# Performance work log

Hardware: AMD Instinct MI355X
Metric: run time of the kernel (lower is better)

The kernel has to match this reference:

```python
import jax, jax.numpy as jnp
import numpy as np
import math

B, S, D, H, R = 4, 2048, 2048, 16, 16
HD = D // H

def setup_inputs() -> dict:
    key = jax.random.key(0)
    ks = jax.random.split(key, 16)
    x = jax.random.normal(ks[0], (B, S, D), dtype=jnp.float32)
    # causal mask: 1 where attendable, 0 where masked (mask==0 -> -1e9)
    mask = jnp.tril(jnp.ones((S, S), dtype=jnp.int32))[None, None, :, :]
    def lin(k):
        return jax.random.normal(k, (D, D), dtype=jnp.float32) / math.sqrt(D)
    def lora(ka, kb):
        A = jax.random.normal(ka, (R, D), dtype=jnp.float32) / math.sqrt(D)
        Bm = jnp.zeros((D, R), dtype=jnp.float32)  # standard LoRA init: B = 0
        return A, Bm
    Aq, Bq = lora(ks[1], ks[2]); Ak, Bk = lora(ks[3], ks[4])
    Av, Bv = lora(ks[5], ks[6]); Ao, Bo = lora(ks[7], ks[8])
    return {"x": x, "mask": mask,
            "Wq": lin(ks[9]), "Aq": Aq, "Bq": Bq,
            "Wk": lin(ks[10]), "Ak": Ak, "Bk": Bk,
            "Wv": lin(ks[11]), "Av": Av, "Bv": Bv,
            "Wo": lin(ks[12]), "Ao": Ao, "Bo": Bo}

def _lora_linear(x, W, A, Bm):
    # y = x @ W^T + (x @ A^T) @ B^T   (LoRA-augmented linear, no bias)
    return x @ W.T + (x @ A.T) @ Bm.T

def reference(x, mask, Wq, Aq, Bq, Wk, Ak, Bk, Wv, Av, Bv, Wo, Ao, Bo):
    b, s, d = x.shape
    def heads(t):
        return t.reshape(b, s, H, HD).transpose(0, 2, 1, 3)  # [B,H,S,HD]
    Q = heads(_lora_linear(x, Wq, Aq, Bq))
    K = heads(_lora_linear(x, Wk, Ak, Bk))
    V = heads(_lora_linear(x, Wv, Av, Bv))
    attn = jnp.einsum('bhqd,bhkd->bhqk', Q, K) / math.sqrt(HD)
    attn = jnp.where(mask == 0, jnp.float32(-1e9), attn)
    attn = jax.nn.softmax(attn, axis=-1)
    out = jnp.einsum('bhqk,bhkd->bhqd', attn, V)  # [B,H,S,HD]
    out = out.transpose(0, 2, 1, 3).reshape(b, s, d)
    return _lora_linear(out, Wo, Ao, Bo)
```

## Files before the change

### kernel.cpp

```cpp
#include <hip/hip_runtime.h>
#include <hip/hip_bf16.h>
#include <stdint.h>


#define L2E 1.4426950408889634f
#define SMSCALE 0.08838834764831845f
#define NEGBIG -3.0e38f

typedef __attribute__((ext_vector_type(4))) float f32x4;
typedef __attribute__((ext_vector_type(16))) float f32x16;
typedef __attribute__((ext_vector_type(8))) __bf16 bfrag;

#if __has_builtin(__builtin_amdgcn_exp2f)
#define EXP2 __builtin_amdgcn_exp2f
#else
#define EXP2 exp2f
#endif

#define DRAIN_VM                                      \
  do {                                                \
    asm volatile("s_waitcnt vmcnt(0)" ::: "memory");  \
    __builtin_amdgcn_sched_barrier(0);                \
  } while (0)

static __device__ __forceinline__ unsigned short f2bf(float f) {
  union { float f; unsigned u; } v; v.f = f;
  unsigned r = v.u + 0x7FFFu + ((v.u >> 16) & 1u);
  return (unsigned short)(r >> 16);
}

static __device__ __forceinline__ void gload16(const void* g, void* l) {
  __builtin_amdgcn_global_load_lds(
      (const __attribute__((address_space(1))) void*)g,
      (__attribute__((address_space(3))) void*)l, 16, 0, 0);
}

struct F4 {
  const float* W[4];
  const float* A[4];
  const float* Bm[4];
};

__global__ __launch_bounds__(256) void k_fold4(F4 f, unsigned short* __restrict__ out) {
  const int y = blockIdx.y;
  const int n = blockIdx.x;
  const int k0 = threadIdx.x * 8;
  const float* W = f.W[y];
  const float* Aa = f.A[y];
  const float* Bm = f.Bm[y];
  const float* wr = W + (size_t)n * 2048 + k0;
  float acc[8];
#pragma unroll
  for (int j = 0; j < 8; ++j) acc[j] = wr[j];
#pragma unroll 4
  for (int r = 0; r < 16; ++r) {
    float b = Bm[n * 16 + r];
    const float* ar = Aa + (size_t)r * 2048 + k0;
#pragma unroll
    for (int j = 0; j < 8; ++j) acc[j] = fmaf(b, ar[j], acc[j]);
  }
  unsigned short o[8];
#pragma unroll
  for (int j = 0; j < 8; ++j) o[j] = f2bf(acc[j]);
  *(uint4*)(out + (((size_t)y * 2048 + n) * 2048) + k0) = *(const uint4*)o;
}

__global__ __launch_bounds__(256) void k_cvt(const float* __restrict__ in,
                                             unsigned short* __restrict__ out) {
  const size_t i = ((size_t)blockIdx.x * 256 + threadIdx.x) * 8;
  unsigned short o[8];
#pragma unroll
  for (int j = 0; j < 8; ++j) o[j] = f2bf(in[i + j]);
  *(uint4*)(out + i) = *(const uint4*)o;
}

template <int MODE>
__global__ __launch_bounds__(512, 2) void k_gemm2(const unsigned short* __restrict__ A,
                                                  const unsigned short* __restrict__ Bw,
                                                  void* __restrict__ Cout, float scale) {
  __shared__ __align__(16) unsigned char lds[131072];
  unsigned char* Al = lds;
  unsigned char* Bl = lds + 65536;
  const int tid = threadIdx.x, ln = tid & 63;
  const int w = tid >> 6, g = ln >> 4, cc = ln & 15;
  const int wm = w >> 2, wn = w & 3;
  const int bid = blockIdx.x;
  const int wg = (bid & 7) * 32 + (bid >> 3);
  const int m0 = (wg >> 3) * 256, n0 = (wg & 7) * 256;

  int soff[2], sdst[2];
#pragma unroll
  for (int i = 0; i < 2; ++i) {
    int cid = i * 512 + tid, r = cid >> 2, p = cid & 3;
    int sc = p ^ ((r >> 1) & 3);
    soff[i] = r * 2048 + sc * 8;
    sdst[i] = cid * 16;
  }
  int aro[8], bro[4];
#pragma unroll
  for (int fm = 0; fm < 8; ++fm) {
    int r = wm * 128 + fm * 16 + cc;
    aro[fm] = r * 64 + ((g ^ ((r >> 1) & 3)) << 4);
  }
#pragma unroll
  for (int fn = 0; fn < 4; ++fn) {
    int r = wn * 64 + fn * 16 + cc;
    bro[fn] = r * 64 + ((g ^ ((r >> 1) & 3)) << 4);
  }

#define STAGE_A(b, kt, h)                                                   \
  do {                                                                      \
    _Pragma("unroll")                                                       \
    for (int i = 0; i < 2; ++i)                                             \
      gload16(A + (size_t)m0 * 2048 + soff[i] + (kt) + (h) * 32,            \
              Al + (b) * 32768 + (h) * 16384 + sdst[i]);                    \
  } while (0)
#define STAGE_B(b, kt, h)                                                   \
  do {                                                                      \
    _Pragma("unroll")                                                       \
    for (int i = 0; i < 2; ++i)                                             \
      gload16(Bw + (size_t)n0 * 2048 + soff[i] + (kt) + (h) * 32,           \
              Bl + (b) * 32768 + (h) * 16384 + sdst[i]);                    \
  } while (0)

  f32x4 acc[8][4] = {};

  STAGE_A(0, 0, 0); STAGE_B(0, 0, 0);
  STAGE_A(0, 0, 1); STAGE_B(0, 0, 1);
  asm volatile("s_waitcnt vmcnt(4)" ::: "memory");
  __builtin_amdgcn_s_barrier();
  __builtin_amdgcn_sched_barrier(0);

  for (int T = 0; T < 32; ++T) {
    const int buf = T & 1;
    const unsigned char* Ab = Al + buf * 32768;
    const unsigned char* Bb = Bl + buf * 32768;
    const int ktn = (T + 1) * 64;
    const bool pf = (T + 1 < 32);
#pragma unroll
    for (int ks = 0; ks < 2; ++ks) {
      bfrag af[8], bf0[2], bf1[2];
#pragma unroll
      for (int fm = 0; fm < 8; ++fm)
        af[fm] = *(const bfrag*)(Ab + ks * 16384 + aro[fm]);
#pragma unroll
      for (int j = 0; j < 2; ++j)
        bf0[j] = *(const bfrag*)(Bb + ks * 16384 + bro[j]);
      if (pf) STAGE_A(buf ^ 1, ktn, ks);
      __builtin_amdgcn_sched_barrier(0);
      __builtin_amdgcn_s_barrier();
      asm volatile("s_waitcnt lgkmcnt(0)" ::: "memory");
      __builtin_amdgcn_sched_barrier(0);
      __builtin_amdgcn_s_setprio(1);
#pragma unroll
      for (int fm = 0; fm < 8; ++fm)
#pragma unroll
        for (int j = 0; j < 2; ++j)
          acc[fm][j] = __builtin_amdgcn_mfma_f32_16x16x32_bf16(af[fm], bf0[j],
                                                               acc[fm][j], 0, 0, 0);
      __builtin_amdgcn_s_setprio(0);
      __builtin_amdgcn_sched_barrier(0);
      __builtin_amdgcn_s_barrier();
#pragma unroll
      for (int j = 0; j < 2; ++j)
        bf1[j] = *(const bfrag*)(Bb + ks * 16384 + bro[2 + j]);
      if (pf) STAGE_B(buf ^ 1, ktn, ks);
      __builtin_amdgcn_sched_barrier(0);
      __builtin_amdgcn_s_barrier();
      asm volatile("s_waitcnt lgkmcnt(0)" ::: "memory");
      __builtin_amdgcn_sched_barrier(0);
      __builtin_amdgcn_s_setprio(1);
#pragma unroll
      for (int fm = 0; fm < 8; ++fm)
#pragma unroll
        for (int j = 0; j < 2; ++j)
          acc[fm][2 + j] = __builtin_amdgcn_mfma_f32_16x16x32_bf16(af[fm], bf1[j],
                                                                   acc[fm][2 + j], 0, 0, 0);
      __builtin_amdgcn_s_setprio(0);
      __builtin_amdgcn_sched_barrier(0);
      if (ks == 0) {
        if (T < 31) asm volatile("s_waitcnt vmcnt(4)" ::: "memory");
        else        asm volatile("s_waitcnt vmcnt(0)" ::: "memory");
      } else {
        if (T < 31) asm volatile("s_waitcnt vmcnt(4)" ::: "memory");
      }
      __builtin_amdgcn_sched_barrier(0);
      __builtin_amdgcn_s_barrier();
    }
  }
#undef STAGE_A
#undef STAGE_B

#pragma unroll
  for (int fm = 0; fm < 8; ++fm)
#pragma unroll
    for (int fn = 0; fn < 4; ++fn)
#pragma unroll
      for (int r = 0; r < 4; ++r) {
        int row = m0 + wm * 128 + fm * 16 + g * 4 + r;
        int col = n0 + wn * 64 + fn * 16 + cc;
        float v = acc[fm][fn][r];
        if (MODE == 0) {
          int b = row >> 11, s = row & 2047, h = col >> 7, hd = col & 127;
          ((unsigned short*)Cout)[(((size_t)b * 16 + h) * 2048 + s) * 128 + hd] =
              f2bf(v * scale);
        } else if (MODE == 2) {
          int b = row >> 11, s = row & 2047, h = col >> 7, hd = col & 127;
          ((unsigned short*)Cout)[(((size_t)b * 16 + h) * 128 + hd) * 2048 + s] =
              f2bf(v);
        } else {
          ((float*)Cout)[(size_t)row * 2048 + col] = v;
        }
      }
}

__global__ __launch_bounds__(512) void k_attn(const unsigned short* __restrict__ Q,
                                              const unsigned short* __restrict__ K,
                                              const unsigned short* __restrict__ Vt,
                                              unsigned short* __restrict__ O) {
  __shared__ __align__(16) unsigned char lds[65536];
  const int tid = threadIdx.x;
  const int ln = tid & 63, w = tid >> 6;
  const int l31 = ln & 31, hi = ln >> 5;
  const int rk = l31 & 15;
  const int bx = blockIdx.x;
  const int qb = 7 - (bx >> 6);
  const int bh = bx & 63;
  const int q0 = qb * 256;
  const size_t base = (size_t)bh * 2048 * 128;
  const unsigned short* Qb = Q + base;
  const unsigned short* Kb = K + base;
  const unsigned short* Vb = Vt + base;

  const int qw0 = q0 + w * 32;
  const int qg = qw0 + l31;

  bfrag qf[8];
#pragma unroll
  for (int dc = 0; dc < 8; ++dc)
    qf[dc] = *(const bfrag*)(Qb + (size_t)qg * 128 + dc * 16 + hi * 8);

  f32x16 o[4] = {};
  float m_r = NEGBIG, l_r = 0.f;

  const int nt = q0 / 64 + 4;

  auto stage = [&](int buf, int k0) {
    unsigned char* Kt = lds + buf * 32768;
    unsigned char* Vl = Kt + 16384;
#pragma unroll
    for (int i = 0; i < 2; ++i) {
      int cid = i * 512 + tid;
      int row = cid >> 4, p = cid & 15, sc = p ^ (row & 15);
      gload16(Kb + (size_t)(k0 + row) * 128 + sc * 8, Kt + cid * 16);
    }
#pragma unroll
    for (int i = 0; i < 2; ++i) {
      int cid = i * 512 + tid;
      int row = cid >> 4, p = cid & 15, sc = p ^ (row & 15);
      int d = (sc >> 3) * 64 + row;
      gload16(Vb + (size_t)d * 2048 + k0 + (sc & 7) * 8, Vl + cid * 16);
    }
  };

  stage(0, 0);
  DRAIN_VM;
  __syncthreads();
  int buf = 0;

  for (int t = 0; t < nt; ++t) {
    const int k0 = t * 64;
    if (t + 1 < nt) stage(buf ^ 1, k0 + 64);

    if (k0 <= qw0 + 31) {
      const unsigned char* Kt = lds + buf * 32768;
      const unsigned char* Vl = Kt + 16384;

      f32x16 s0 = {}, s1 = {};
#pragma unroll
      for (int dc = 0; dc < 8; ++dc) {
        int c = dc * 2 + hi;
        bfrag ka = *(const bfrag*)(Kt + (size_t)l31 * 256 + ((c ^ rk) << 4));
        bfrag kb2 = *(const bfrag*)(Kt + (size_t)(32 + l31) * 256 + ((c ^ rk) << 4));
        s0 = __builtin_amdgcn_mfma_f32_32x32x16_bf16(ka, qf[dc], s0, 0, 0, 0);
        s1 = __builtin_amdgcn_mfma_f32_32x32x16_bf16(kb2, qf[dc], s1, 0, 0, 0);
      }

      if (k0 + 63 > qw0) {
#pragma unroll
        for (int r = 0; r < 16; ++r) {
          int ko = (r & 3) + 8 * (r >> 2) + 4 * hi;
          if (k0 + ko > qg) s0[r] = NEGBIG;
          if (k0 + 32 + ko > qg) s1[r] = NEGBIG;
        }
      }

      float pmax = s0[0];
#pragma unroll
      for (int r = 1; r < 16; ++r) pmax = fmaxf(pmax, s0[r]);
#pragma unroll
      for (int r = 0; r < 16; ++r) pmax = fmaxf(pmax, s1[r]);
      pmax = fmaxf(pmax, __shfl_xor(pmax, 32));

      if (!__all(pmax - m_r <= 12.f)) {
        float mn = fmaxf(m_r, pmax);
        float al = EXP2(m_r - mn);
        l_r *= al;
#pragma unroll
        for (int db = 0; db < 4; ++db)
#pragma unroll
          for (int r = 0; r < 16; ++r) o[db][r] *= al;
        m_r = mn;
      }

      unsigned qd0[8], qd1[8];
      float rs = 0.f;
#pragma unroll
      for (int s = 0; s < 4; ++s) {
        float p0 = EXP2(s0[4 * s + 0] - m_r), p1 = EXP2(s0[4 * s + 1] - m_r);
        float p2 = EXP2(s0[4 * s + 2] - m_r), p3 = EXP2(s0[4 * s + 3] - m_r);
        rs += (p0 + p1) + (p2 + p3);
        qd0[2 * s] = (unsigned)f2bf(p0) | ((unsigned)f2bf(p1) << 16);
        qd0[2 * s + 1] = (unsigned)f2bf(p2) | ((unsigned)f2bf(p3) << 16);
      }
#pragma unroll
      for (int s = 0; s < 4; ++s) {
        float p0 = EXP2(s1[4 * s + 0] - m_r), p1 = EXP2(s1[4 * s + 1] - m_r);
        float p2 = EXP2(s1[4 * s + 2] - m_r), p3 = EXP2(s1[4 * s + 3] - m_r);
        rs += (p0 + p1) + (p2 + p3);
        qd1[2 * s] = (unsigned)f2bf(p0) | ((unsigned)f2bf(p1) << 16);
        qd1[2 * s + 1] = (unsigned)f2bf(p2) | ((unsigned)f2bf(p3) << 16);
      }
      rs += __shfl_xor(rs, 32);
      l_r += rs;

#define PVSTEP(QD, B0, KC)                                                    \
  do {                                                                        \
    unsigned e0 = QD[B0], e1 = QD[B0 + 1], x0 = QD[B0 + 2], x1 = QD[B0 + 3];  \
    unsigned kp0 = hi ? x0 : e0, kp1 = hi ? x1 : e1;                          \
    unsigned sd0 = hi ? e0 : x0, sd1 = hi ? e1 : x1;                          \
    unsigned rc0 = (unsigned)__shfl_xor((int)sd0, 32);                        \
    unsigned rc1 = (unsigned)__shfl_xor((int)sd1, 32);                        \
    unsigned pw[4];                                                           \
    pw[0] = hi ? rc0 : kp0; pw[1] = hi ? rc1 : kp1;                           \
    pw[2] = hi ? kp0 : rc0; pw[3] = hi ? kp1 : rc1;                           \
    bfrag pf = *(bfrag*)pw;                                                   \
    _Pragma("unroll")                                                         \
    for (int db = 0; db < 4; ++db) {                                          \
      int c = (db >> 1) * 8 + KC * 2 + hi;                                    \
      bfrag vf = *(const bfrag*)(Vl + (size_t)((db & 1) * 32 + l31) * 256 +   \
                                 ((c ^ rk) << 4));                            \
      o[db] = __builtin_amdgcn_mfma_f32_32x32x16_bf16(vf, pf, o[db], 0, 0, 0);\
    }                                                                         \
  } while (0)

      PVSTEP(qd0, 0, 0);
      PVSTEP(qd0, 4, 1);
      PVSTEP(qd1, 0, 2);
      PVSTEP(qd1, 4, 3);
#undef PVSTEP
    }
    DRAIN_VM;
    __syncthreads();
    buf ^= 1;
  }

  float invl = 1.0f / l_r;
  const int b_ = bh >> 4, h_ = bh & 15;
#pragma unroll
  for (int ph = 0; ph < 2; ++ph) {
    if ((w >> 2) == ph) {
      unsigned char* ep = lds + (w & 3) * 8704;
#pragma unroll
      for (int db = 0; db < 4; ++db)
#pragma unroll
        for (int s = 0; s < 4; ++s) {
          int d0 = db * 32 + 8 * s + 4 * hi;
          float v0 = o[db][4 * s] * invl, v1 = o[db][4 * s + 1] * invl;
          float v2 = o[db][4 * s + 2] * invl, v3 = o[db][4 * s + 3] * invl;
          uint2 pw;
          pw.x = (unsigned)f2bf(v0) | ((unsigned)f2bf(v1) << 16);
          pw.y = (unsigned)f2bf(v2) | ((unsigned)f2bf(v3) << 16);
          *(uint2*)(ep + l31 * 272 + d0 * 2) = pw;
        }
    }
    __syncthreads();
    if ((w >> 2) == ph) {
      const unsigned char* ep = lds + (w & 3) * 8704;
#pragma unroll
      for (int i = 0; i < 8; ++i) {
        int cid = i * 64 + ln;
        int q = cid >> 4, ch = cid & 15;
        uint4 val = *(const uint4*)(ep + q * 272 + ch * 16);
        *(uint4*)(O + ((size_t)(b_ * 2048 + q0 + w * 32 + q)) * 2048 +
                  h_ * 128 + ch * 8) = val;
      }
    }
    __syncthreads();
  }
}

extern "C" void kernel_launch(void* const* d_in, const int* in_sizes, int n_in,
                              void* d_out, int out_size, void* d_ws, size_t ws_size,
                              hipStream_t stream) {
  (void)in_sizes; (void)n_in; (void)out_size; (void)ws_size;
  const float* x  = (const float*)d_in[0];

  char* ws = (char*)d_ws;
  unsigned short* xbf  = (unsigned short*)ws;
  unsigned short* Wall = (unsigned short*)(ws + (size_t)33554432);
  unsigned short* Qb   = (unsigned short*)(ws + (size_t)67108864);
  unsigned short* Kb   = Qb + 16777216;
  unsigned short* Vtb  = Kb + 16777216;
  unsigned short* AO   = xbf;

  F4 f;
  f.W[0] = (const float*)d_in[2];  f.A[0] = (const float*)d_in[3];  f.Bm[0] = (const float*)d_in[4];
  f.W[1] = (const float*)d_in[5];  f.A[1] = (const float*)d_in[6];  f.Bm[1] = (const float*)d_in[7];
  f.W[2] = (const float*)d_in[8];  f.A[2] = (const float*)d_in[9];  f.Bm[2] = (const float*)d_in[10];
  f.W[3] = (const float*)d_in[11]; f.A[3] = (const float*)d_in[12]; f.Bm[3] = (const float*)d_in[13];

  k_fold4<<<dim3(2048, 4), 256, 0, stream>>>(f, Wall);
  k_cvt<<<8192, 256, 0, stream>>>(x, xbf);

  k_gemm2<0><<<256, 512, 0, stream>>>(xbf, Wall, Qb, SMSCALE * L2E);
  k_gemm2<0><<<256, 512, 0, stream>>>(xbf, Wall + 4194304, Kb, 1.0f);
  k_gemm2<2><<<256, 512, 0, stream>>>(xbf, Wall + 8388608, Vtb, 1.0f);

  k_attn<<<512, 512, 0, stream>>>(Qb, Kb, Vtb, AO);

  k_gemm2<1><<<256, 512, 0, stream>>>(AO, Wall + 12582912, d_out, 1.0f);
}
```

Measured before the change: 410.2 us.

## Shrink GEMM tile to 256x128 with smaller LDS for higher occupancy

The projection GEMM changes from a 256x256 tile with a 64-wide K step and 128 KB of LDS to a 256x128 tile with a 32-wide K step and 48 KB of LDS. Launch bounds rise to 4 blocks per CU and the grid doubles to 512 blocks. The hand-tuned interleaved staging with partial vmcnt waits is replaced by a simple double-buffered loop that fully drains loads and syncs every iteration. The aim is more resident waves to hide latency, at the cost of less data reuse per tile, more loop iterations with barriers, and weaker overlap of loads with MFMA.

After: 439.9 us. 1.07x slower.

```diff
diff --git a/kernel.cpp b/kernel.cpp
--- a/kernel.cpp
+++ b/kernel.cpp
@@ -75,130 +75,95 @@
 }
 
 template <int MODE>
-__global__ __launch_bounds__(512, 2) void k_gemm2(const unsigned short* __restrict__ A,
+__global__ __launch_bounds__(512, 4) void k_gemm4(const unsigned short* __restrict__ A,
                                                   const unsigned short* __restrict__ Bw,
                                                   void* __restrict__ Cout, float scale) {
-  __shared__ __align__(16) unsigned char lds[131072];
+  __shared__ __align__(16) unsigned char lds[49152];
   unsigned char* Al = lds;
-  unsigned char* Bl = lds + 65536;
+  unsigned char* Bl = lds + 32768;
   const int tid = threadIdx.x, ln = tid & 63;
   const int w = tid >> 6, g = ln >> 4, cc = ln & 15;
   const int wm = w >> 2, wn = w & 3;
   const int bid = blockIdx.x;
-  const int wg = (bid & 7) * 32 + (bid >> 3);
-  const int m0 = (wg >> 3) * 256, n0 = (wg & 7) * 256;
-
-  int soff[2], sdst[2];
+  const int wg = (bid & 7) * 64 + (bid >> 3);
+  const int m0 = (wg >> 4) * 256, n0 = (wg & 15) * 128;
+
+  int soffA[2], sdstA[2];
 #pragma unroll
   for (int i = 0; i < 2; ++i) {
     int cid = i * 512 + tid, r = cid >> 2, p = cid & 3;
     int sc = p ^ ((r >> 1) & 3);
-    soff[i] = r * 2048 + sc * 8;
-    sdst[i] = cid * 16;
-  }
-  int aro[8], bro[4];
+    soffA[i] = r * 2048 + sc * 8;
+    sdstA[i] = cid * 16;
+  }
+  int soffB, sdstB;
+  {
+    int r = tid >> 2, p = tid & 3;
+    int sc = p ^ ((r >> 1) & 3);
+    soffB = r * 2048 + sc * 8;
+    sdstB = tid * 16;
+  }
+  int aro[8], bro[2];
 #pragma unroll
   for (int fm = 0; fm < 8; ++fm) {
     int r = wm * 128 + fm * 16 + cc;
     aro[fm] = r * 64 + ((g ^ ((r >> 1) & 3)) << 4);
   }
 #pragma unroll
-  for (int fn = 0; fn < 4; ++fn) {
-    int r = wn * 64 + fn * 16 + cc;
+  for (int fn = 0; fn < 2; ++fn) {
+    int r = wn * 32 + fn * 16 + cc;
     bro[fn] = r * 64 + ((g ^ ((r >> 1) & 3)) << 4);
   }
 
-#define STAGE_A(b, kt, h)                                                   \
+#define STAGE(b, kt)                                                        \
   do {                                                                      \
     _Pragma("unroll")                                                       \
     for (int i = 0; i < 2; ++i)                                             \
-      gload16(A + (size_t)m0 * 2048 + soff[i] + (kt) + (h) * 32,            \
-              Al + (b) * 32768 + (h) * 16384 + sdst[i]);                    \
+      gload16(A + (size_t)m0 * 2048 + soffA[i] + (kt),                      \
+              Al + (b) * 16384 + sdstA[i]);                                 \
+    gload16(Bw + (size_t)n0 * 2048 + soffB + (kt),                          \
+            Bl + (b) * 8192 + sdstB);                                       \
   } while (0)
-#define STAGE_B(b, kt, h)                                                   \
-  do {                                                                      \
-    _Pragma("unroll")                                                       \
-    for (int i = 0; i < 2; ++i)                                             \
-      gload16(Bw + (size_t)n0 * 2048 + soff[i] + (kt) + (h) * 32,           \
-              Bl + (b) * 32768 + (h) * 16384 + sdst[i]);                    \
-  } while (0)
-
-  f32x4 acc[8][4] = {};
-
-  STAGE_A(0, 0, 0); STAGE_B(0, 0, 0);
-  STAGE_A(0, 0, 1); STAGE_B(0, 0, 1);
-  asm volatile("s_waitcnt vmcnt(4)" ::: "memory");
-  __builtin_amdgcn_s_barrier();
-  __builtin_amdgcn_sched_barrier(0);
-
-  for (int T = 0; T < 32; ++T) {
+
+  f32x4 acc[8][2] = {};
+
+  STAGE(0, 0);
+  DRAIN_VM;
+  __syncthreads();
+
+  for (int T = 0; T < 64; ++T) {
     const int buf = T & 1;
-    const unsigned char* Ab = Al + buf * 32768;
-    const unsigned char* Bb = Bl + buf * 32768;
-    const int ktn = (T + 1) * 64;
-    const bool pf = (T + 1 < 32);
-#pragma unroll
-    for (int ks = 0; ks < 2; ++ks) {
-      bfrag af[8], bf0[2], bf1[2];
-#pragma unroll
-      for (int fm = 0; fm < 8; ++fm)
-        af[fm] = *(const bfrag*)(Ab + ks * 16384 + aro[fm]);
-#pragma unroll
-      for (int j = 0; j < 2; ++j)
-        bf0[j] = *(const bfrag*)(Bb + ks * 16384 + bro[j]);
-      if (pf) STAGE_A(buf ^ 1, ktn, ks);
-      __builtin_amdgcn_sched_barrier(0);
-      __builtin_amdgcn_s_barrier();
-      asm volatile("s_waitcnt lgkmcnt(0)" ::: "memory");
-      __builtin_amdgcn_sched_barrier(0);
-      __builtin_amdgcn_s_setprio(1);
-#pragma unroll
-      for (int fm = 0; fm < 8; ++fm)
-#pragma unroll
-        for (int j = 0; j < 2; ++j)
-          acc[fm][j] = __builtin_amdgcn_mfma_f32_16x16x32_bf16(af[fm], bf0[j],
-                                                               acc[fm][j], 0, 0, 0);
-      __builtin_amdgcn_s_setprio(0);
-      __builtin_amdgcn_sched_barrier(0);
-      __builtin_amdgcn_s_barrier();
-#pragma unroll
-      for (int j = 0; j < 2; ++j)
-        bf1[j] = *(const bfrag*)(Bb + ks * 16384 + bro[2 + j]);
-      if (pf) STAGE_B(buf ^ 1, ktn, ks);
-      __builtin_amdgcn_sched_barrier(0);
-      __builtin_amdgcn_s_barrier();
-      asm volatile("s_waitcnt lgkmcnt(0)" ::: "memory");
-      __builtin_amdgcn_sched_barrier(0);
-      __builtin_amdgcn_s_setprio(1);
-#pragma unroll
-      for (int fm = 0; fm < 8; ++fm)
-#pragma unroll
-        for (int j = 0; j < 2; ++j)
-          acc[fm][2 + j] = __builtin_amdgcn_mfma_f32_16x16x32_bf16(af[fm], bf1[j],
-                                                                   acc[fm][2 + j], 0, 0, 0);
-      __builtin_amdgcn_s_setprio(0);
-      __builtin_amdgcn_sched_barrier(0);
-      if (ks == 0) {
-        if (T < 31) asm volatile("s_waitcnt vmcnt(4)" ::: "memory");
-        else        asm volatile("s_waitcnt vmcnt(0)" ::: "memory");
-      } else {
-        if (T < 31) asm volatile("s_waitcnt vmcnt(4)" ::: "memory");
-      }
-      __builtin_amdgcn_sched_barrier(0);
-      __builtin_amdgcn_s_barrier();
-    }
-  }
-#undef STAGE_A
-#undef STAGE_B
+    if (T < 63) STAGE(buf ^ 1, (T + 1) * 32);
+    const unsigned char* Ab = Al + buf * 16384;
+    const unsigned char* Bb = Bl + buf * 8192;
+    bfrag af[8], bf[2];
+#pragma unroll
+    for (int fm = 0; fm < 8; ++fm)
+      af[fm] = *(const bfrag*)(Ab + aro[fm]);
+#pragma unroll
+    for (int fn = 0; fn < 2; ++fn)
+      bf[fn] = *(const bfrag*)(Bb + bro[fn]);
+    __builtin_amdgcn_s_setprio(1);
+#pragma unroll
+    for (int fm = 0; fm < 8; ++fm)
+#pragma unroll
+      for (int fn = 0; fn < 2; ++fn)
+        acc[fm][fn] = __builtin_amdgcn_mfma_f32_16x16x32_bf16(af[fm], bf[fn],
+                                                              acc[fm][fn], 0, 0, 0);
+    __builtin_amdgcn_s_setprio(0);
+    DRAIN_VM;
+    __syncthreads();
+  }
+#undef STAGE
 
 #pragma unroll
   for (int fm = 0; fm < 8; ++fm)
 #pragma unroll
-    for (int fn = 0; fn < 4; ++fn)
+    for (int fn = 0; fn < 2; ++fn)
 #pragma unroll
       for (int r = 0; r < 4; ++r) {
         int row = m0 + wm * 128 + fm * 16 + g * 4 + r;
-        int col = n0 + wn * 64 + fn * 16 + cc;
+        int col = n0 + wn * 32 + fn * 16 + cc;
         float v = acc[fm][fn][r];
         if (MODE == 0) {
           int b = row >> 11, s = row & 2047, h = col >> 7, hd = col & 127;
@@ -423,11 +388,11 @@
   k_fold4<<<dim3(2048, 4), 256, 0, stream>>>(f, Wall);
   k_cvt<<<8192, 256, 0, stream>>>(x, xbf);
 
-  k_gemm2<0><<<256, 512, 0, stream>>>(xbf, Wall, Qb, SMSCALE * L2E);
-  k_gemm2<0><<<256, 512, 0, stream>>>(xbf, Wall + 4194304, Kb, 1.0f);
-  k_gemm2<2><<<256, 512, 0, stream>>>(xbf, Wall + 8388608, Vtb, 1.0f);
+  k_gemm4<0><<<512, 512, 0, stream>>>(xbf, Wall, Qb, SMSCALE * L2E);
+  k_gemm4<0><<<512, 512, 0, stream>>>(xbf, Wall + 4194304, Kb, 1.0f);
+  k_gemm4<2><<<512, 512, 0, stream>>>(xbf, Wall + 8388608, Vtb, 1.0f);
 
   k_attn<<<512, 512, 0, stream>>>(Qb, Kb, Vtb, AO);
 
-  k_gemm2<1><<<256, 512, 0, stream>>>(AO, Wall + 12582912, d_out, 1.0f);
-}
+  k_gemm4<1><<<512, 512, 0, stream>>>(AO, Wall + 12582912, d_out, 1.0f);
+}
```

## Use persistent atomic work queue for causal attention and merge prep kernels

Applied to the files above, without the earlier changes.

The attention kernel becomes persistent: 384 blocks pull (q-block, head) work items from a global atomic counter, longest causal rows first. The goal is to balance the triangular workload across CUs instead of relying on hardware block dispatch. The weight fold and x-to-bf16 conversion are merged into one launch to cut launch overhead, and the GEMM wait logic is simplified without changing its behavior. The trade-off is an extra memset, an atomic plus block barrier per work item, and a fixed grid size that may not match the CU count.

After: 428.3 us. +4.4%, slower.

```diff
diff --git a/kernel.cpp b/kernel.cpp
--- a/kernel.cpp
+++ b/kernel.cpp
@@ -41,9 +41,20 @@
   const float* Bm[4];
 };
 
-__global__ __launch_bounds__(256) void k_fold4(F4 f, unsigned short* __restrict__ out) {
-  const int y = blockIdx.y;
-  const int n = blockIdx.x;
+__global__ __launch_bounds__(256) void k_prep(F4 f, const float* __restrict__ x,
+                                              unsigned short* __restrict__ xbf,
+                                              unsigned short* __restrict__ Wall) {
+  const int bid = blockIdx.x;
+  if (bid < 8192) {
+    const size_t i = ((size_t)bid * 256 + threadIdx.x) * 8;
+    unsigned short o[8];
+#pragma unroll
+    for (int j = 0; j < 8; ++j) o[j] = f2bf(x[i + j]);
+    *(uint4*)(xbf + i) = *(const uint4*)o;
+    return;
+  }
+  const int y = (bid - 8192) >> 11;
+  const int n = (bid - 8192) & 2047;
   const int k0 = threadIdx.x * 8;
   const float* W = f.W[y];
   const float* Aa = f.A[y];
@@ -62,16 +73,7 @@
   unsigned short o[8];
 #pragma unroll
   for (int j = 0; j < 8; ++j) o[j] = f2bf(acc[j]);
-  *(uint4*)(out + (((size_t)y * 2048 + n) * 2048) + k0) = *(const uint4*)o;
-}
-
-__global__ __launch_bounds__(256) void k_cvt(const float* __restrict__ in,
-                                             unsigned short* __restrict__ out) {
-  const size_t i = ((size_t)blockIdx.x * 256 + threadIdx.x) * 8;
-  unsigned short o[8];
-#pragma unroll
-  for (int j = 0; j < 8; ++j) o[j] = f2bf(in[i + j]);
-  *(uint4*)(out + i) = *(const uint4*)o;
+  *(uint4*)(Wall + (((size_t)y * 2048 + n) * 2048) + k0) = *(const uint4*)o;
 }
 
 template <int MODE>
@@ -178,12 +180,8 @@
                                                                    acc[fm][2 + j], 0, 0, 0);
       __builtin_amdgcn_s_setprio(0);
       __builtin_amdgcn_sched_barrier(0);
-      if (ks == 0) {
-        if (T < 31) asm volatile("s_waitcnt vmcnt(4)" ::: "memory");
-        else        asm volatile("s_waitcnt vmcnt(0)" ::: "memory");
-      } else {
-        if (T < 31) asm volatile("s_waitcnt vmcnt(4)" ::: "memory");
-      }
+      if (T < 31) asm volatile("s_waitcnt vmcnt(4)" ::: "memory");
+      else if (ks == 0) asm volatile("s_waitcnt vmcnt(0)" ::: "memory");
       __builtin_amdgcn_sched_barrier(0);
       __builtin_amdgcn_s_barrier();
     }
@@ -217,122 +215,129 @@
 __global__ __launch_bounds__(512) void k_attn(const unsigned short* __restrict__ Q,
                                               const unsigned short* __restrict__ K,
                                               const unsigned short* __restrict__ Vt,
-                                              unsigned short* __restrict__ O) {
+                                              unsigned short* __restrict__ O,
+                                              int* __restrict__ ctr) {
   __shared__ __align__(16) unsigned char lds[65536];
+  __shared__ int s_item;
   const int tid = threadIdx.x;
   const int ln = tid & 63, w = tid >> 6;
   const int l31 = ln & 31, hi = ln >> 5;
   const int rk = l31 & 15;
-  const int bx = blockIdx.x;
-  const int qb = 7 - (bx >> 6);
-  const int bh = bx & 63;
-  const int q0 = qb * 256;
-  const size_t base = (size_t)bh * 2048 * 128;
-  const unsigned short* Qb = Q + base;
-  const unsigned short* Kb = K + base;
-  const unsigned short* Vb = Vt + base;
-
-  const int qw0 = q0 + w * 32;
-  const int qg = qw0 + l31;
-
-  bfrag qf[8];
-#pragma unroll
-  for (int dc = 0; dc < 8; ++dc)
-    qf[dc] = *(const bfrag*)(Qb + (size_t)qg * 128 + dc * 16 + hi * 8);
-
-  f32x16 o[4] = {};
-  float m_r = NEGBIG, l_r = 0.f;
-
-  const int nt = q0 / 64 + 4;
-
-  auto stage = [&](int buf, int k0) {
-    unsigned char* Kt = lds + buf * 32768;
-    unsigned char* Vl = Kt + 16384;
-#pragma unroll
-    for (int i = 0; i < 2; ++i) {
-      int cid = i * 512 + tid;
-      int row = cid >> 4, p = cid & 15, sc = p ^ (row & 15);
-      gload16(Kb + (size_t)(k0 + row) * 128 + sc * 8, Kt + cid * 16);
-    }
-#pragma unroll
-    for (int i = 0; i < 2; ++i) {
-      int cid = i * 512 + tid;
-      int row = cid >> 4, p = cid & 15, sc = p ^ (row & 15);
-      int d = (sc >> 3) * 64 + row;
-      gload16(Vb + (size_t)d * 2048 + k0 + (sc & 7) * 8, Vl + cid * 16);
-    }
-  };
-
-  stage(0, 0);
-  DRAIN_VM;
-  __syncthreads();
-  int buf = 0;
-
-  for (int t = 0; t < nt; ++t) {
-    const int k0 = t * 64;
-    if (t + 1 < nt) stage(buf ^ 1, k0 + 64);
-
-    if (k0 <= qw0 + 31) {
-      const unsigned char* Kt = lds + buf * 32768;
-      const unsigned char* Vl = Kt + 16384;
-
-      f32x16 s0 = {}, s1 = {};
-#pragma unroll
-      for (int dc = 0; dc < 8; ++dc) {
-        int c = dc * 2 + hi;
-        bfrag ka = *(const bfrag*)(Kt + (size_t)l31 * 256 + ((c ^ rk) << 4));
-        bfrag kb2 = *(const bfrag*)(Kt + (size_t)(32 + l31) * 256 + ((c ^ rk) << 4));
-        s0 = __builtin_amdgcn_mfma_f32_32x32x16_bf16(ka, qf[dc], s0, 0, 0, 0);
-        s1 = __builtin_amdgcn_mfma_f32_32x32x16_bf16(kb2, qf[dc], s1, 0, 0, 0);
-      }
-
-      if (k0 + 63 > qw0) {
-#pragma unroll
-        for (int r = 0; r < 16; ++r) {
-          int ko = (r & 3) + 8 * (r >> 2) + 4 * hi;
-          if (k0 + ko > qg) s0[r] = NEGBIG;
-          if (k0 + 32 + ko > qg) s1[r] = NEGBIG;
-        }
-      }
-
-      float pmax = s0[0];
-#pragma unroll
-      for (int r = 1; r < 16; ++r) pmax = fmaxf(pmax, s0[r]);
-#pragma unroll
-      for (int r = 0; r < 16; ++r) pmax = fmaxf(pmax, s1[r]);
-      pmax = fmaxf(pmax, __shfl_xor(pmax, 32));
-
-      if (!__all(pmax - m_r <= 12.f)) {
-        float mn = fmaxf(m_r, pmax);
-        float al = EXP2(m_r - mn);
-        l_r *= al;
-#pragma unroll
-        for (int db = 0; db < 4; ++db)
-#pragma unroll
-          for (int r = 0; r < 16; ++r) o[db][r] *= al;
-        m_r = mn;
-      }
-
-      unsigned qd0[8], qd1[8];
-      float rs = 0.f;
-#pragma unroll
-      for (int s = 0; s < 4; ++s) {
-        float p0 = EXP2(s0[4 * s + 0] - m_r), p1 = EXP2(s0[4 * s + 1] - m_r);
-        float p2 = EXP2(s0[4 * s + 2] - m_r), p3 = EXP2(s0[4 * s + 3] - m_r);
-        rs += (p0 + p1) + (p2 + p3);
-        qd0[2 * s] = (unsigned)f2bf(p0) | ((unsigned)f2bf(p1) << 16);
-        qd0[2 * s + 1] = (unsigned)f2bf(p2) | ((unsigned)f2bf(p3) << 16);
-      }
-#pragma unroll
-      for (int s = 0; s < 4; ++s) {
-        float p0 = EXP2(s1[4 * s + 0] - m_r), p1 = EXP2(s1[4 * s + 1] - m_r);
-        float p2 = EXP2(s1[4 * s + 2] - m_r), p3 = EXP2(s1[4 * s + 3] - m_r);
-        rs += (p0 + p1) + (p2 + p3);
-        qd1[2 * s] = (unsigned)f2bf(p0) | ((unsigned)f2bf(p1) << 16);
-        qd1[2 * s + 1] = (unsigned)f2bf(p2) | ((unsigned)f2bf(p3) << 16);
-      }
-      rs += __shfl_xor(rs, 32);
-      l_r += rs;
+
+  for (;;) {
+    if (tid == 0) s_item = atomicAdd(ctr, 1);
+    __syncthreads();
+    const int item = s_item;
+    if (item >= 512) return;
+    const int qb = 7 - (item >> 6);
+    const int bh = item & 63;
+    const int q0 = qb * 256;
+    const size_t base = (size_t)bh * 2048 * 128;
+    const unsigned short* Qb = Q + base;
+    const unsigned short* Kb = K + base;
+    const unsigned short* Vb = Vt + base;
+
+    const int qw0 = q0 + w * 32;
+    const int qg = qw0 + l31;
+
+    bfrag qf[8];
+#pragma unroll
+    for (int dc = 0; dc < 8; ++dc)
+      qf[dc] = *(const bfrag*)(Qb + (size_t)qg * 128 + dc * 16 + hi * 8);
+
+    f32x16 o[4] = {};
+    float m_r = NEGBIG, l_r = 0.f;
+
+    const int nt = q0 / 64 + 4;
+
+    auto stage = [&](int buf, int k0) {
+      unsigned char* Kt = lds + buf * 32768;
+      unsigned char* Vl = Kt + 16384;
+#pragma unroll
+      for (int i = 0; i < 2; ++i) {
+        int cid = i * 512 + tid;
+        int row = cid >> 4, p = cid & 15, sc = p ^ (row & 15);
+        gload16(Kb + (size_t)(k0 + row) * 128 + sc * 8, Kt + cid * 16);
+      }
+#pragma unroll
+      for (int i = 0; i < 2; ++i) {
+        int cid = i * 512 + tid;
+        int row = cid >> 4, p = cid & 15, sc = p ^ (row & 15);
+        int d = (sc >> 3) * 64 + row;
+        gload16(Vb + (size_t)d * 2048 + k0 + (sc & 7) * 8, Vl + cid * 16);
+      }
+    };
+
+    stage(0, 0);
+    DRAIN_VM;
+    __syncthreads();
+    int buf = 0;
+
+    for (int t = 0; t < nt; ++t) {
+      const int k0 = t * 64;
+      if (t + 1 < nt) stage(buf ^ 1, k0 + 64);
+
+      if (k0 <= qw0 + 31) {
+        const unsigned char* Kt = lds + buf * 32768;
+        const unsigned char* Vl = Kt + 16384;
+
+        f32x16 s0 = {}, s1 = {};
+#pragma unroll
+        for (int dc = 0; dc < 8; ++dc) {
+          int c = dc * 2 + hi;
+          bfrag ka = *(const bfrag*)(Kt + (size_t)l31 * 256 + ((c ^ rk) << 4));
+          bfrag kb2 = *(const bfrag*)(Kt + (size_t)(32 + l31) * 256 + ((c ^ rk) << 4));
+          s0 = __builtin_amdgcn_mfma_f32_32x32x16_bf16(ka, qf[dc], s0, 0, 0, 0);
+          s1 = __builtin_amdgcn_mfma_f32_32x32x16_bf16(kb2, qf[dc], s1, 0, 0, 0);
+        }
+
+        if (k0 + 63 > qw0) {
+#pragma unroll
+          for (int r = 0; r < 16; ++r) {
+            int ko = (r & 3) + 8 * (r >> 2) + 4 * hi;
+            if (k0 + ko > qg) s0[r] = NEGBIG;
+            if (k0 + 32 + ko > qg) s1[r] = NEGBIG;
+          }
+        }
+
+        float pmax = s0[0];
+#pragma unroll
+        for (int r = 1; r < 16; ++r) pmax = fmaxf(pmax, s0[r]);
+#pragma unroll
+        for (int r = 0; r < 16; ++r) pmax = fmaxf(pmax, s1[r]);
+        pmax = fmaxf(pmax, __shfl_xor(pmax, 32));
+
+        if (!__all(pmax - m_r <= 12.f)) {
+          float mn = fmaxf(m_r, pmax);
+          float al = EXP2(m_r - mn);
+          l_r *= al;
+#pragma unroll
+          for (int db = 0; db < 4; ++db)
+#pragma unroll
+            for (int r = 0; r < 16; ++r) o[db][r] *= al;
+          m_r = mn;
+        }
+
+        unsigned qd0[8], qd1[8];
+        float rs = 0.f;
+#pragma unroll
+        for (int s = 0; s < 4; ++s) {
+          float p0 = EXP2(s0[4 * s + 0] - m_r), p1 = EXP2(s0[4 * s + 1] - m_r);
+          float p2 = EXP2(s0[4 * s + 2] - m_r), p3 = EXP2(s0[4 * s + 3] - m_r);
+          rs += (p0 + p1) + (p2 + p3);
+          qd0[2 * s] = (unsigned)f2bf(p0) | ((unsigned)f2bf(p1) << 16);
+          qd0[2 * s + 1] = (unsigned)f2bf(p2) | ((unsigned)f2bf(p3) << 16);
+        }
+#pragma unroll
+        for (int s = 0; s < 4; ++s) {
+          float p0 = EXP2(s1[4 * s + 0] - m_r), p1 = EXP2(s1[4 * s + 1] - m_r);
+          float p2 = EXP2(s1[4 * s + 2] - m_r), p3 = EXP2(s1[4 * s + 3] - m_r);
+          rs += (p0 + p1) + (p2 + p3);
+          qd1[2 * s] = (unsigned)f2bf(p0) | ((unsigned)f2bf(p1) << 16);
+          qd1[2 * s + 1] = (unsigned)f2bf(p2) | ((unsigned)f2bf(p3) << 16);
+        }
+        rs += __shfl_xor(rs, 32);
+        l_r += rs;
 
 #define PVSTEP(QD, B0, KC)                                                    \
   do {                                                                        \
@@ -354,49 +359,50 @@
     }                                                                         \
   } while (0)
 
-      PVSTEP(qd0, 0, 0);
-      PVSTEP(qd0, 4, 1);
-      PVSTEP(qd1, 0, 2);
-      PVSTEP(qd1, 4, 3);
+        PVSTEP(qd0, 0, 0);
+        PVSTEP(qd0, 4, 1);
+        PVSTEP(qd1, 0, 2);
+        PVSTEP(qd1, 4, 3);
 #undef PVSTEP
+      }
+      DRAIN_VM;
+      __syncthreads();
+      buf ^= 1;
     }
-    DRAIN_VM;
-    __syncthreads();
-    buf ^= 1;
-  }
-
-  float invl = 1.0f / l_r;
-  const int b_ = bh >> 4, h_ = bh & 15;
-#pragma unroll
-  for (int ph = 0; ph < 2; ++ph) {
-    if ((w >> 2) == ph) {
-      unsigned char* ep = lds + (w & 3) * 8704;
-#pragma unroll
-      for (int db = 0; db < 4; ++db)
-#pragma unroll
-        for (int s = 0; s < 4; ++s) {
-          int d0 = db * 32 + 8 * s + 4 * hi;
-          float v0 = o[db][4 * s] * invl, v1 = o[db][4 * s + 1] * invl;
-          float v2 = o[db][4 * s + 2] * invl, v3 = o[db][4 * s + 3] * invl;
-          uint2 pw;
-          pw.x = (unsigned)f2bf(v0) | ((unsigned)f2bf(v1) << 16);
-          pw.y = (unsigned)f2bf(v2) | ((unsigned)f2bf(v3) << 16);
-          *(uint2*)(ep + l31 * 272 + d0 * 2) = pw;
-        }
+
+    float invl = 1.0f / l_r;
+    const int b_ = bh >> 4, h_ = bh & 15;
+#pragma unroll
+    for (int ph = 0; ph < 2; ++ph) {
+      if ((w >> 2) == ph) {
+        unsigned char* ep = lds + (w & 3) * 8704;
+#pragma unroll
+        for (int db = 0; db < 4; ++db)
+#pragma unroll
+          for (int s = 0; s < 4; ++s) {
+            int d0 = db * 32 + 8 * s + 4 * hi;
+            float v0 = o[db][4 * s] * invl, v1 = o[db][4 * s + 1] * invl;
+            float v2 = o[db][4 * s + 2] * invl, v3 = o[db][4 * s + 3] * invl;
+            uint2 pw;
+            pw.x = (unsigned)f2bf(v0) | ((unsigned)f2bf(v1) << 16);
+            pw.y = (unsigned)f2bf(v2) | ((unsigned)f2bf(v3) << 16);
+            *(uint2*)(ep + l31 * 272 + d0 * 2) = pw;
+          }
+      }
+      __syncthreads();
+      if ((w >> 2) == ph) {
+        const unsigned char* ep = lds + (w & 3) * 8704;
+#pragma unroll
+        for (int i = 0; i < 8; ++i) {
+          int cid = i * 64 + ln;
+          int q = cid >> 4, ch = cid & 15;
+          uint4 val = *(const uint4*)(ep + q * 272 + ch * 16);
+          *(uint4*)(O + ((size_t)(b_ * 2048 + q0 + w * 32 + q)) * 2048 +
+                    h_ * 128 + ch * 8) = val;
+        }
+      }
+      __syncthreads();
     }
-    __syncthreads();
-    if ((w >> 2) == ph) {
-      const unsigned char* ep = lds + (w & 3) * 8704;
-#pragma unroll
-      for (int i = 0; i < 8; ++i) {
-        int cid = i * 64 + ln;
-        int q = cid >> 4, ch = cid & 15;
-        uint4 val = *(const uint4*)(ep + q * 272 + ch * 16);
-        *(uint4*)(O + ((size_t)(b_ * 2048 + q0 + w * 32 + q)) * 2048 +
-                  h_ * 128 + ch * 8) = val;
-      }
-    }
-    __syncthreads();
   }
 }
 
@@ -413,6 +419,7 @@
   unsigned short* Kb   = Qb + 16777216;
   unsigned short* Vtb  = Kb + 16777216;
   unsigned short* AO   = xbf;
+  int* ctr = (int*)(ws + (size_t)167772160);
 
   F4 f;
   f.W[0] = (const float*)d_in[2];  f.A[0] = (const float*)d_in[3];  f.Bm[0] = (const float*)d_in[4];
@@ -420,14 +427,14 @@
   f.W[2] = (const float*)d_in[8];  f.A[2] = (const float*)d_in[9];  f.Bm[2] = (const float*)d_in[10];
   f.W[3] = (const float*)d_in[11]; f.A[3] = (const float*)d_in[12]; f.Bm[3] = (const float*)d_in[13];
 
-  k_fold4<<<dim3(2048, 4), 256, 0, stream>>>(f, Wall);
-  k_cvt<<<8192, 256, 0, stream>>>(x, xbf);
+  hipMemsetAsync(ctr, 0, 4, stream);
+  k_prep<<<16384, 256, 0, stream>>>(f, x, xbf, Wall);
 
   k_gemm2<0><<<256, 512, 0, stream>>>(xbf, Wall, Qb, SMSCALE * L2E);
   k_gemm2<0><<<256, 512, 0, stream>>>(xbf, Wall + 4194304, Kb, 1.0f);
   k_gemm2<2><<<256, 512, 0, stream>>>(xbf, Wall + 8388608, Vtb, 1.0f);
 
-  k_attn<<<512, 512, 0, stream>>>(Qb, Kb, Vtb, AO);
+  k_attn<<<384, 512, 0, stream>>>(Qb, Kb, Vtb, AO, ctr);
 
   k_gemm2<1><<<256, 512, 0, stream>>>(AO, Wall + 12582912, d_out, 1.0f);
 }
```
